# Performance work log

Hardware: AMD Instinct MI355X
Metric: run time of the kernel (lower is better)

The kernel has to match this reference:

```python
import jax, jax.numpy as jnp
import numpy as np

EPSILON = 1e-08

def setup_inputs() -> dict:
    key0 = jax.random.key(0)
    kq, kk, kv = jax.random.split(key0, 3)
    B, Q, H, D = 64, 16, 1, 64
    KV, DV = 16384, 64
    query = jax.random.normal(kq, (B, Q, H, D), dtype=jnp.float32)
    key = jax.random.normal(kk, (B, KV, H, D), dtype=jnp.float32)
    value = jax.random.normal(kv, (B, KV, H, DV), dtype=jnp.float32)
    return {"query": query, "key": key, "value": value}

def reference(query, key, value):
    # InvertedDotProductAttention(norm_type='mean', multi_head=False)
    d = query.shape[-1]
    q = query / jnp.sqrt(jnp.asarray(d, dtype=query.dtype))
    # logits: [b, h, q, k]
    attn = jnp.einsum('bqhd,bkhd->bhqk', q, key)
    # inverted attention: softmax over the query axis (-2)
    attn = jax.nn.softmax(attn, axis=-2)
    # renormalize_keys=True (norm_type == 'mean'): normalize over key axis
    attn = attn / (jnp.sum(attn, axis=-1, keepdims=True) + EPSILON)
    out = jnp.einsum('bhqk,bkhd->bqhd', attn, value)
    # multi_head=False -> squeeze the (singleton) heads axis
    return jnp.squeeze(out, axis=-2)
```

## Files before the change

kernel.cpp:

```cpp
#include <hip/hip_runtime.h>

namespace {

typedef float f32x4 __attribute__((ext_vector_type(4)));
typedef short bf16x8 __attribute__((ext_vector_type(8)));

constexpr int Bn = 64, QN = 16, Dn = 64, DVn = 64, KVn = 16384;
constexpr int MAX_SPLITS = 32;
constexpr int TILE    = 64;
constexpr int THREADS = 256;
constexpr int AP   = 68;
constexpr int VROW = 160;

constexpr float SCALE = 0.125f * 1.4426950408889634f;

__device__ __forceinline__ unsigned cvt_pk_bf16(float a, float b) {
    unsigned r;
    asm("v_cvt_pk_bf16_f32 %0, %1, %2" : "=v"(r) : "v"(a), "v"(b));
    return r;
}

union FragU { unsigned u[4]; bf16x8 v; };

__device__ __forceinline__ void split8(const float x[8], bf16x8& hi, bf16x8& lo) {
    FragU uh, ul;
#pragma unroll
    for (int p = 0; p < 4; ++p) {
        const float a = x[2 * p], b2 = x[2 * p + 1];
        const unsigned h = cvt_pk_bf16(a, b2);
        uh.u[p] = h;
        const float ha = __uint_as_float(h << 16);
        const float hb = __uint_as_float(h & 0xffff0000u);
        ul.u[p] = cvt_pk_bf16(a - ha, b2 - hb);
    }
    hi = uh.v; lo = ul.v;
}

__global__ __launch_bounds__(THREADS, 4)
void inv_attn_part(const float* __restrict__ query,
                   const float* __restrict__ key,
                   const float* __restrict__ value,
                   float* __restrict__ pout,
                   float* __restrict__ pden,
                   int ntiles)
{
    __shared__ __align__(16) float a_s[2][QN * AP];
    __shared__ __align__(16) char  vT[2][DVn * VROW];
    __shared__ float den_buf[4][QN];

    const int tid  = threadIdx.x;
    const int lane = tid & 63;
    const int w    = tid >> 6;
    const int l15  = lane & 15;
    const int g    = lane >> 4;
    const int spl  = blockIdx.x;
    const int splits = gridDim.x;
    const int b    = blockIdx.y;
    const int kt0  = spl * ntiles * TILE;

    bf16x8 qhi[2], qlo[2];
    {
        const float* qp = query + ((size_t)b * QN + l15) * Dn + g * 8;
#pragma unroll
        for (int ks = 0; ks < 2; ++ks) {
            const float4 u0 = *reinterpret_cast<const float4*>(qp + ks * 32);
            const float4 u1 = *reinterpret_cast<const float4*>(qp + ks * 32 + 4);
            float x[8] = { u0.x * SCALE, u0.y * SCALE, u0.z * SCALE, u0.w * SCALE,
                           u1.x * SCALE, u1.y * SCALE, u1.z * SCALE, u1.w * SCALE };
            split8(x, qhi[ks], qlo[ks]);
        }
    }

    f32x4 oacc = {0.f, 0.f, 0.f, 0.f};
    float den0 = 0.f, den1 = 0.f, den2 = 0.f, den3 = 0.f;

    const int vkey = tid >> 4;
    const int vdv0 = (tid & 15) * 4;
    const int vsw  = ((tid & 15) & 7) << 4;

    const float* kbase = key   + ((size_t)b * KVn + kt0 + w * 16 + l15) * Dn + g * 8;
    const float* vbase = value + ((size_t)b * KVn + kt0 + vkey) * Dn + vdv0;

    for (int t = 0; t < ntiles; ++t) {
        const int buf = t & 1;

        float4 vv[4];
#pragma unroll
        for (int i = 0; i < 4; ++i)
            vv[i] = *reinterpret_cast<const float4*>(vbase + ((size_t)t * TILE + 16 * i) * Dn);
#pragma unroll
        for (int i = 0; i < 4; ++i) {
            const int kk = vkey + 16 * i;
#pragma unroll
            for (int j = 0; j < 4; ++j) {
                const float xv = (j == 0) ? vv[i].x : (j == 1) ? vv[i].y
                                : (j == 2) ? vv[i].z : vv[i].w;
                const unsigned uu = cvt_pk_bf16(xv, xv);
                *reinterpret_cast<short*>(&vT[buf][(vdv0 + j) * VROW + ((2 * kk) ^ vsw)]) =
                    (short)uu;
            }
        }

        f32x4 sacc = {0.f, 0.f, 0.f, 0.f};
#pragma unroll
        for (int ks = 0; ks < 2; ++ks) {
            const float4 ka = *reinterpret_cast<const float4*>(kbase + (size_t)t * TILE * Dn + ks * 32);
            const float4 kb = *reinterpret_cast<const float4*>(kbase + (size_t)t * TILE * Dn + ks * 32 + 4);
            float x[8] = { ka.x, ka.y, ka.z, ka.w, kb.x, kb.y, kb.z, kb.w };
            bf16x8 khi, klo;
            split8(x, khi, klo);
            sacc = __builtin_amdgcn_mfma_f32_16x16x32_bf16(qhi[ks], khi, sacc, 0, 0, 0);
            sacc = __builtin_amdgcn_mfma_f32_16x16x32_bf16(qhi[ks], klo, sacc, 0, 0, 0);
            sacc = __builtin_amdgcn_mfma_f32_16x16x32_bf16(qlo[ks], khi, sacc, 0, 0, 0);
        }

        float m = fmaxf(fmaxf(sacc[0], sacc[1]), fmaxf(sacc[2], sacc[3]));
        m = fmaxf(m, __shfl_xor(m, 16, 64));
        m = fmaxf(m, __shfl_xor(m, 32, 64));
        float p0 = exp2f(sacc[0] - m), p1 = exp2f(sacc[1] - m);
        float p2 = exp2f(sacc[2] - m), p3 = exp2f(sacc[3] - m);
        float s4 = p0 + p1 + p2 + p3;
        s4 += __shfl_xor(s4, 16, 64);
        s4 += __shfl_xor(s4, 32, 64);
        const float inv = 1.0f / s4;
        p0 *= inv; p1 *= inv; p2 *= inv; p3 *= inv;
        const int kloc = w * 16 + l15;
        a_s[buf][(g * 4 + 0) * AP + kloc] = p0;
        a_s[buf][(g * 4 + 1) * AP + kloc] = p1;
        a_s[buf][(g * 4 + 2) * AP + kloc] = p2;
        a_s[buf][(g * 4 + 3) * AP + kloc] = p3;
        den0 += p0; den1 += p1; den2 += p2; den3 += p3;

        __syncthreads();

#pragma unroll
        for (int ks = 0; ks < 2; ++ks) {
            const int base = ks * 32 + g * 8;
            const float4 a0 = *reinterpret_cast<const float4*>(&a_s[buf][l15 * AP + base]);
            const float4 a1 = *reinterpret_cast<const float4*>(&a_s[buf][l15 * AP + base + 4]);
            FragU ua;
            ua.u[0] = cvt_pk_bf16(a0.x, a0.y);
            ua.u[1] = cvt_pk_bf16(a0.z, a0.w);
            ua.u[2] = cvt_pk_bf16(a1.x, a1.y);
            ua.u[3] = cvt_pk_bf16(a1.z, a1.w);
            const int dv = w * 16 + l15;
            const int gran = (((ks * 4 + g) ^ ((dv >> 2) & 7)) << 4);
            const bf16x8 vf = *reinterpret_cast<const bf16x8*>(&vT[buf][dv * VROW + gran]);
            oacc = __builtin_amdgcn_mfma_f32_16x16x32_bf16(ua.v, vf, oacc, 0, 0, 0);
        }
    }

    const size_t obase = (((size_t)b * splits + spl) * QN) * DVn;
    const int dv = w * 16 + l15;
    pout[obase + (g * 4 + 0) * DVn + dv] = oacc[0];
    pout[obase + (g * 4 + 1) * DVn + dv] = oacc[1];
    pout[obase + (g * 4 + 2) * DVn + dv] = oacc[2];
    pout[obase + (g * 4 + 3) * DVn + dv] = oacc[3];

#pragma unroll
    for (int off = 1; off < 16; off <<= 1) {
        den0 += __shfl_xor(den0, off, 64);
        den1 += __shfl_xor(den1, off, 64);
        den2 += __shfl_xor(den2, off, 64);
        den3 += __shfl_xor(den3, off, 64);
    }
    if (l15 == 0) {
        den_buf[w][g * 4 + 0] = den0;
        den_buf[w][g * 4 + 1] = den1;
        den_buf[w][g * 4 + 2] = den2;
        den_buf[w][g * 4 + 3] = den3;
    }
    __syncthreads();
    if (tid < QN) {
        const float d = den_buf[0][tid] + den_buf[1][tid] + den_buf[2][tid] + den_buf[3][tid];
        pden[((size_t)b * splits + spl) * QN + tid] = d;
    }
}

__global__ __launch_bounds__(256)
void inv_attn_reduce(const float* __restrict__ pout,
                     const float* __restrict__ pden,
                     float* __restrict__ out,
                     int splits)
{
    const int gid = blockIdx.x * blockDim.x + threadIdx.x;
    const int dv = gid & 63;
    const int q  = (gid >> 6) & (QN - 1);
    const int b  = gid >> 10;
    float sum = 0.f, den = 0.f;
#pragma unroll 8
    for (int sp = 0; sp < splits; ++sp) {
        sum += pout[(((size_t)b * splits + sp) * QN + q) * DVn + dv];
        den += pden[((size_t)b * splits + sp) * QN + q];
    }
    out[gid] = sum / (den + 1e-8f);
}

}

extern "C" void kernel_launch(void* const* d_in, const int* in_sizes, int n_in,
                              void* d_out, int out_size, void* d_ws, size_t ws_size,
                              hipStream_t stream) {
    const float* query = (const float*)d_in[0];
    const float* key   = (const float*)d_in[1];
    const float* value = (const float*)d_in[2];
    float* out = (float*)d_out;

    int splits = MAX_SPLITS;
    auto need = [](int s) {
        return (size_t)Bn * s * QN * DVn * sizeof(float)
             + (size_t)Bn * s * QN * sizeof(float);
    };
    while (splits > 1 && need(splits) > ws_size) splits >>= 1;

    float* pout = (float*)d_ws;
    float* pden = pout + (size_t)Bn * splits * QN * DVn;

    const int ntiles = KVn / (splits * TILE);

    dim3 grid1(splits, Bn);
    inv_attn_part<<<grid1, THREADS, 0, stream>>>(query, key, value, pout, pden, ntiles);

    const int total = Bn * QN * DVn;
    inv_attn_reduce<<<total / 256, 256, 0, stream>>>(pout, pden, out, splits);
}
```

Baseline: 105.5 us.

## Make each wave process independent key tiles and drop block-wide barriers

Each wavefront now handles its own pair of 16-key groups per iteration and computes P·V with only a per-wave LDS transpose of the probabilities. V is loaded straight from global memory in MFMA fragment layout, which removes the shared V transpose and the per-tile __syncthreads. Per-wave partial outputs and denominators are written out, so the reduce kernel sums four times as many partials. This removes barrier and LDS staging costs, but the V loads become strided scalar loads and the partial-buffer traffic grows.

Measured after the change: 123.8 us. 17.3% more time.

```diff
diff --git a/kernel.cpp b/kernel.cpp
--- a/kernel.cpp
+++ b/kernel.cpp
@@ -7,10 +7,9 @@
 
 constexpr int Bn = 64, QN = 16, Dn = 64, DVn = 64, KVn = 16384;
 constexpr int MAX_SPLITS = 32;
-constexpr int TILE    = 64;
+constexpr int TILE = 64;
 constexpr int THREADS = 256;
-constexpr int AP   = 68;
-constexpr int VROW = 160;
+constexpr int PTP = 20;
 
 constexpr float SCALE = 0.125f * 1.4426950408889634f;
 
@@ -22,18 +21,47 @@
 
 union FragU { unsigned u[4]; bf16x8 v; };
 
-__device__ __forceinline__ void split8(const float x[8], bf16x8& hi, bf16x8& lo) {
+__device__ __forceinline__ void split8(const float* x, bf16x8& hi, bf16x8& lo) {
     FragU uh, ul;
 #pragma unroll
     for (int p = 0; p < 4; ++p) {
-        const float a = x[2 * p], b2 = x[2 * p + 1];
-        const unsigned h = cvt_pk_bf16(a, b2);
+        const float a = x[2 * p], b = x[2 * p + 1];
+        const unsigned h = cvt_pk_bf16(a, b);
         uh.u[p] = h;
         const float ha = __uint_as_float(h << 16);
         const float hb = __uint_as_float(h & 0xffff0000u);
-        ul.u[p] = cvt_pk_bf16(a - ha, b2 - hb);
+        ul.u[p] = cvt_pk_bf16(a - ha, b - hb);
     }
     hi = uh.v; lo = ul.v;
+}
+
+__device__ __forceinline__ f32x4 qk_softmax(const float* kp,
+                                            const bf16x8 qhi[2],
+                                            const bf16x8 qlo[2]) {
+    f32x4 sacc = {0.f, 0.f, 0.f, 0.f};
+#pragma unroll
+    for (int ks = 0; ks < 2; ++ks) {
+        const float4 a = *reinterpret_cast<const float4*>(kp + ks * 32);
+        const float4 b = *reinterpret_cast<const float4*>(kp + ks * 32 + 4);
+        float x[8] = {a.x, a.y, a.z, a.w, b.x, b.y, b.z, b.w};
+        bf16x8 khi, klo;
+        split8(x, khi, klo);
+        sacc = __builtin_amdgcn_mfma_f32_16x16x32_bf16(qhi[ks], khi, sacc, 0, 0, 0);
+        sacc = __builtin_amdgcn_mfma_f32_16x16x32_bf16(qhi[ks], klo, sacc, 0, 0, 0);
+        sacc = __builtin_amdgcn_mfma_f32_16x16x32_bf16(qlo[ks], khi, sacc, 0, 0, 0);
+    }
+    float m = fmaxf(fmaxf(sacc[0], sacc[1]), fmaxf(sacc[2], sacc[3]));
+    m = fmaxf(m, __shfl_xor(m, 16, 64));
+    m = fmaxf(m, __shfl_xor(m, 32, 64));
+    f32x4 pr;
+    pr[0] = exp2f(sacc[0] - m); pr[1] = exp2f(sacc[1] - m);
+    pr[2] = exp2f(sacc[2] - m); pr[3] = exp2f(sacc[3] - m);
+    float s = pr[0] + pr[1] + pr[2] + pr[3];
+    s += __shfl_xor(s, 16, 64);
+    s += __shfl_xor(s, 32, 64);
+    const float inv = 1.0f / s;
+    pr[0] *= inv; pr[1] *= inv; pr[2] *= inv; pr[3] *= inv;
+    return pr;
 }
 
 __global__ __launch_bounds__(THREADS, 4)
@@ -42,21 +70,19 @@
                    const float* __restrict__ value,
                    float* __restrict__ pout,
                    float* __restrict__ pden,
-                   int ntiles)
+                   int npairs)
 {
-    __shared__ __align__(16) float a_s[2][QN * AP];
-    __shared__ __align__(16) char  vT[2][DVn * VROW];
-    __shared__ float den_buf[4][QN];
-
-    const int tid  = threadIdx.x;
+    __shared__ __align__(16) float pT[4][32 * PTP];
+
+    const int tid = threadIdx.x;
     const int lane = tid & 63;
-    const int w    = tid >> 6;
-    const int l15  = lane & 15;
-    const int g    = lane >> 4;
-    const int spl  = blockIdx.x;
+    const int w = tid >> 6;
+    const int l15 = lane & 15;
+    const int g = lane >> 4;
+    const int spl = blockIdx.x;
     const int splits = gridDim.x;
-    const int b    = blockIdx.y;
-    const int kt0  = spl * ntiles * TILE;
+    const int b = blockIdx.y;
+    const int kt0 = spl * (npairs * 2 * TILE) + w * 16;
 
     bf16x8 qhi[2], qlo[2];
     {
@@ -65,115 +91,82 @@
         for (int ks = 0; ks < 2; ++ks) {
             const float4 u0 = *reinterpret_cast<const float4*>(qp + ks * 32);
             const float4 u1 = *reinterpret_cast<const float4*>(qp + ks * 32 + 4);
-            float x[8] = { u0.x * SCALE, u0.y * SCALE, u0.z * SCALE, u0.w * SCALE,
-                           u1.x * SCALE, u1.y * SCALE, u1.z * SCALE, u1.w * SCALE };
+            float x[8] = {u0.x * SCALE, u0.y * SCALE, u0.z * SCALE, u0.w * SCALE,
+                          u1.x * SCALE, u1.y * SCALE, u1.z * SCALE, u1.w * SCALE};
             split8(x, qhi[ks], qlo[ks]);
         }
     }
 
-    f32x4 oacc = {0.f, 0.f, 0.f, 0.f};
-    float den0 = 0.f, den1 = 0.f, den2 = 0.f, den3 = 0.f;
-
-    const int vkey = tid >> 4;
-    const int vdv0 = (tid & 15) * 4;
-    const int vsw  = ((tid & 15) & 7) << 4;
-
-    const float* kbase = key   + ((size_t)b * KVn + kt0 + w * 16 + l15) * Dn + g * 8;
-    const float* vbase = value + ((size_t)b * KVn + kt0 + vkey) * Dn + vdv0;
-
-    for (int t = 0; t < ntiles; ++t) {
-        const int buf = t & 1;
-
-        float4 vv[4];
-#pragma unroll
-        for (int i = 0; i < 4; ++i)
-            vv[i] = *reinterpret_cast<const float4*>(vbase + ((size_t)t * TILE + 16 * i) * Dn);
-#pragma unroll
-        for (int i = 0; i < 4; ++i) {
-            const int kk = vkey + 16 * i;
-#pragma unroll
-            for (int j = 0; j < 4; ++j) {
-                const float xv = (j == 0) ? vv[i].x : (j == 1) ? vv[i].y
-                                : (j == 2) ? vv[i].z : vv[i].w;
-                const unsigned uu = cvt_pk_bf16(xv, xv);
-                *reinterpret_cast<short*>(&vT[buf][(vdv0 + j) * VROW + ((2 * kk) ^ vsw)]) =
-                    (short)uu;
-            }
-        }
-
-        f32x4 sacc = {0.f, 0.f, 0.f, 0.f};
-#pragma unroll
-        for (int ks = 0; ks < 2; ++ks) {
-            const float4 ka = *reinterpret_cast<const float4*>(kbase + (size_t)t * TILE * Dn + ks * 32);
-            const float4 kb = *reinterpret_cast<const float4*>(kbase + (size_t)t * TILE * Dn + ks * 32 + 4);
-            float x[8] = { ka.x, ka.y, ka.z, ka.w, kb.x, kb.y, kb.z, kb.w };
-            bf16x8 khi, klo;
-            split8(x, khi, klo);
-            sacc = __builtin_amdgcn_mfma_f32_16x16x32_bf16(qhi[ks], khi, sacc, 0, 0, 0);
-            sacc = __builtin_amdgcn_mfma_f32_16x16x32_bf16(qhi[ks], klo, sacc, 0, 0, 0);
-            sacc = __builtin_amdgcn_mfma_f32_16x16x32_bf16(qlo[ks], khi, sacc, 0, 0, 0);
-        }
-
-        float m = fmaxf(fmaxf(sacc[0], sacc[1]), fmaxf(sacc[2], sacc[3]));
-        m = fmaxf(m, __shfl_xor(m, 16, 64));
-        m = fmaxf(m, __shfl_xor(m, 32, 64));
-        float p0 = exp2f(sacc[0] - m), p1 = exp2f(sacc[1] - m);
-        float p2 = exp2f(sacc[2] - m), p3 = exp2f(sacc[3] - m);
-        float s4 = p0 + p1 + p2 + p3;
-        s4 += __shfl_xor(s4, 16, 64);
-        s4 += __shfl_xor(s4, 32, 64);
-        const float inv = 1.0f / s4;
-        p0 *= inv; p1 *= inv; p2 *= inv; p3 *= inv;
-        const int kloc = w * 16 + l15;
-        a_s[buf][(g * 4 + 0) * AP + kloc] = p0;
-        a_s[buf][(g * 4 + 1) * AP + kloc] = p1;
-        a_s[buf][(g * 4 + 2) * AP + kloc] = p2;
-        a_s[buf][(g * 4 + 3) * AP + kloc] = p3;
-        den0 += p0; den1 += p1; den2 += p2; den3 += p3;
-
-        __syncthreads();
-
-#pragma unroll
-        for (int ks = 0; ks < 2; ++ks) {
-            const int base = ks * 32 + g * 8;
-            const float4 a0 = *reinterpret_cast<const float4*>(&a_s[buf][l15 * AP + base]);
-            const float4 a1 = *reinterpret_cast<const float4*>(&a_s[buf][l15 * AP + base + 4]);
-            FragU ua;
-            ua.u[0] = cvt_pk_bf16(a0.x, a0.y);
-            ua.u[1] = cvt_pk_bf16(a0.z, a0.w);
-            ua.u[2] = cvt_pk_bf16(a1.x, a1.y);
-            ua.u[3] = cvt_pk_bf16(a1.z, a1.w);
-            const int dv = w * 16 + l15;
-            const int gran = (((ks * 4 + g) ^ ((dv >> 2) & 7)) << 4);
-            const bf16x8 vf = *reinterpret_cast<const bf16x8*>(&vT[buf][dv * VROW + gran]);
-            oacc = __builtin_amdgcn_mfma_f32_16x16x32_bf16(ua.v, vf, oacc, 0, 0, 0);
-        }
-    }
-
-    const size_t obase = (((size_t)b * splits + spl) * QN) * DVn;
-    const int dv = w * 16 + l15;
-    pout[obase + (g * 4 + 0) * DVn + dv] = oacc[0];
-    pout[obase + (g * 4 + 1) * DVn + dv] = oacc[1];
-    pout[obase + (g * 4 + 2) * DVn + dv] = oacc[2];
-    pout[obase + (g * 4 + 3) * DVn + dv] = oacc[3];
+    const float* kp = key + ((size_t)b * KVn + kt0 + l15) * Dn + g * 8;
+    const float* vp = value + ((size_t)b * KVn + kt0 + (g & 1) * 8 + (g >> 1) * TILE) * Dn + l15;
+    float* pTw = &pT[w][0];
+
+    f32x4 o0 = {0.f,0.f,0.f,0.f}, o1 = {0.f,0.f,0.f,0.f},
+          o2 = {0.f,0.f,0.f,0.f}, o3 = {0.f,0.f,0.f,0.f};
+    f32x4 den = {0.f,0.f,0.f,0.f};
+
+    for (int p = 0; p < npairs; ++p) {
+        const f32x4 pA = qk_softmax(kp, qhi, qlo);
+        const f32x4 pB = qk_softmax(kp + 64 * Dn, qhi, qlo);
+        den[0] += pA[0] + pB[0]; den[1] += pA[1] + pB[1];
+        den[2] += pA[2] + pB[2]; den[3] += pA[3] + pB[3];
+
+        *reinterpret_cast<f32x4*>(&pTw[l15 * PTP + g * 4]) = pA;
+        *reinterpret_cast<f32x4*>(&pTw[(16 + l15) * PTP + g * 4]) = pB;
+
+        float ax[8];
+#pragma unroll
+        for (int j = 0; j < 8; ++j) ax[j] = pTw[(g * 8 + j) * PTP + l15];
+        FragU ua;
+        ua.u[0] = cvt_pk_bf16(ax[0], ax[1]);
+        ua.u[1] = cvt_pk_bf16(ax[2], ax[3]);
+        ua.u[2] = cvt_pk_bf16(ax[4], ax[5]);
+        ua.u[3] = cvt_pk_bf16(ax[6], ax[7]);
+
+#define PV_CHUNK(c, oc) {                                                     \
+        float vx[8];                                                          \
+        _Pragma("unroll")                                                     \
+        for (int j = 0; j < 8; ++j) vx[j] = vp[j * Dn + (c) * 16];            \
+        FragU uv;                                                             \
+        uv.u[0] = cvt_pk_bf16(vx[0], vx[1]);                                  \
+        uv.u[1] = cvt_pk_bf16(vx[2], vx[3]);                                  \
+        uv.u[2] = cvt_pk_bf16(vx[4], vx[5]);                                  \
+        uv.u[3] = cvt_pk_bf16(vx[6], vx[7]);                                  \
+        oc = __builtin_amdgcn_mfma_f32_16x16x32_bf16(ua.v, uv.v, oc, 0, 0, 0); }
+        PV_CHUNK(0, o0)
+        PV_CHUNK(1, o1)
+        PV_CHUNK(2, o2)
+        PV_CHUNK(3, o3)
+#undef PV_CHUNK
+
+        kp += 128 * Dn;
+        vp += 128 * Dn;
+    }
+
+    const int s4 = spl * 4 + w;
+    const size_t obase = (((size_t)b * (splits * 4) + s4) * QN) * DVn;
+#pragma unroll
+    for (int r = 0; r < 4; ++r) {
+        const int q = g * 4 + r;
+        pout[obase + q * DVn +  0 + l15] = o0[r];
+        pout[obase + q * DVn + 16 + l15] = o1[r];
+        pout[obase + q * DVn + 32 + l15] = o2[r];
+        pout[obase + q * DVn + 48 + l15] = o3[r];
+    }
 
 #pragma unroll
     for (int off = 1; off < 16; off <<= 1) {
-        den0 += __shfl_xor(den0, off, 64);
-        den1 += __shfl_xor(den1, off, 64);
-        den2 += __shfl_xor(den2, off, 64);
-        den3 += __shfl_xor(den3, off, 64);
+        den[0] += __shfl_xor(den[0], off, 64);
+        den[1] += __shfl_xor(den[1], off, 64);
+        den[2] += __shfl_xor(den[2], off, 64);
+        den[3] += __shfl_xor(den[3], off, 64);
     }
     if (l15 == 0) {
-        den_buf[w][g * 4 + 0] = den0;
-        den_buf[w][g * 4 + 1] = den1;
-        den_buf[w][g * 4 + 2] = den2;
-        den_buf[w][g * 4 + 3] = den3;
-    }
-    __syncthreads();
-    if (tid < QN) {
-        const float d = den_buf[0][tid] + den_buf[1][tid] + den_buf[2][tid] + den_buf[3][tid];
-        pden[((size_t)b * splits + spl) * QN + tid] = d;
+        const size_t dbase = ((size_t)b * (splits * 4) + s4) * QN + g * 4;
+        pden[dbase + 0] = den[0];
+        pden[dbase + 1] = den[1];
+        pden[dbase + 2] = den[2];
+        pden[dbase + 3] = den[3];
     }
 }
 
@@ -181,17 +174,17 @@
 void inv_attn_reduce(const float* __restrict__ pout,
                      const float* __restrict__ pden,
                      float* __restrict__ out,
-                     int splits)
+                     int splits4)
 {
     const int gid = blockIdx.x * blockDim.x + threadIdx.x;
     const int dv = gid & 63;
     const int q  = (gid >> 6) & (QN - 1);
     const int b  = gid >> 10;
     float sum = 0.f, den = 0.f;
-#pragma unroll 8
-    for (int sp = 0; sp < splits; ++sp) {
-        sum += pout[(((size_t)b * splits + sp) * QN + q) * DVn + dv];
-        den += pden[((size_t)b * splits + sp) * QN + q];
+#pragma unroll 4
+    for (int sp = 0; sp < splits4; ++sp) {
+        sum += pout[(((size_t)b * splits4 + sp) * QN + q) * DVn + dv];
+        den += pden[((size_t)b * splits4 + sp) * QN + q];
     }
     out[gid] = sum / (den + 1e-8f);
 }
@@ -208,19 +201,19 @@
 
     int splits = MAX_SPLITS;
     auto need = [](int s) {
-        return (size_t)Bn * s * QN * DVn * sizeof(float)
-             + (size_t)Bn * s * QN * sizeof(float);
+        return (size_t)Bn * s * 4 * QN * DVn * sizeof(float)
+             + (size_t)Bn * s * 4 * QN * sizeof(float);
     };
     while (splits > 1 && need(splits) > ws_size) splits >>= 1;
 
     float* pout = (float*)d_ws;
-    float* pden = pout + (size_t)Bn * splits * QN * DVn;
-
-    const int ntiles = KVn / (splits * TILE);
+    float* pden = pout + (size_t)Bn * (splits * 4) * QN * DVn;
+
+    const int npairs = KVn / (splits * TILE * 2);
 
     dim3 grid1(splits, Bn);
-    inv_attn_part<<<grid1, THREADS, 0, stream>>>(query, key, value, pout, pden, ntiles);
+    inv_attn_part<<<grid1, THREADS, 0, stream>>>(query, key, value, pout, pden, npairs);
 
     const int total = Bn * QN * DVn;
-    inv_attn_reduce<<<total / 256, 256, 0, stream>>>(pout, pden, out, splits);
-}
+    inv_attn_reduce<<<total / 256, 256, 0, stream>>>(pout, pden, out, splits * 4);
+}
```

## Prefetch next K/V tile into registers and write per-wave partial denominators

Applied to the files above, without the earlier changes.

The main loop now loads the next tile's key and value float4s into a second register set before the current tile's QK MFMA and softmax, alternating two register buffers through a two-way unrolled loop. This hides global-load latency behind compute. The block-level denominator reduction (shared buffer plus a final __syncthreads) is replaced by each wave writing its own partial sums. The reduce kernel sums four times as many denominator entries. Register pressure rises with the duplicated K/V buffers, and the unroll assumes ntiles is even.

New measurement: 121.2 us. +14.9%, slower.

```diff
diff --git a/kernel.cpp b/kernel.cpp
--- a/kernel.cpp
+++ b/kernel.cpp
@@ -7,7 +7,7 @@
 
 constexpr int Bn = 64, QN = 16, Dn = 64, DVn = 64, KVn = 16384;
 constexpr int MAX_SPLITS = 32;
-constexpr int TILE    = 64;
+constexpr int TILE = 64;
 constexpr int THREADS = 256;
 constexpr int AP   = 68;
 constexpr int VROW = 160;
@@ -22,16 +22,16 @@
 
 union FragU { unsigned u[4]; bf16x8 v; };
 
-__device__ __forceinline__ void split8(const float x[8], bf16x8& hi, bf16x8& lo) {
+__device__ __forceinline__ void split8(const float* x, bf16x8& hi, bf16x8& lo) {
     FragU uh, ul;
 #pragma unroll
     for (int p = 0; p < 4; ++p) {
-        const float a = x[2 * p], b2 = x[2 * p + 1];
-        const unsigned h = cvt_pk_bf16(a, b2);
+        const float a = x[2 * p], b = x[2 * p + 1];
+        const unsigned h = cvt_pk_bf16(a, b);
         uh.u[p] = h;
         const float ha = __uint_as_float(h << 16);
         const float hb = __uint_as_float(h & 0xffff0000u);
-        ul.u[p] = cvt_pk_bf16(a - ha, b2 - hb);
+        ul.u[p] = cvt_pk_bf16(a - ha, b - hb);
     }
     hi = uh.v; lo = ul.v;
 }
@@ -46,7 +46,6 @@
 {
     __shared__ __align__(16) float a_s[2][QN * AP];
     __shared__ __align__(16) char  vT[2][DVn * VROW];
-    __shared__ float den_buf[4][QN];
 
     const int tid  = threadIdx.x;
     const int lane = tid & 63;
@@ -65,48 +64,61 @@
         for (int ks = 0; ks < 2; ++ks) {
             const float4 u0 = *reinterpret_cast<const float4*>(qp + ks * 32);
             const float4 u1 = *reinterpret_cast<const float4*>(qp + ks * 32 + 4);
-            float x[8] = { u0.x * SCALE, u0.y * SCALE, u0.z * SCALE, u0.w * SCALE,
-                           u1.x * SCALE, u1.y * SCALE, u1.z * SCALE, u1.w * SCALE };
+            float x[8] = {u0.x * SCALE, u0.y * SCALE, u0.z * SCALE, u0.w * SCALE,
+                          u1.x * SCALE, u1.y * SCALE, u1.z * SCALE, u1.w * SCALE};
             split8(x, qhi[ks], qlo[ks]);
         }
     }
 
-    f32x4 oacc = {0.f, 0.f, 0.f, 0.f};
-    float den0 = 0.f, den1 = 0.f, den2 = 0.f, den3 = 0.f;
-
+    const float* kbase = key + ((size_t)b * KVn + kt0 + w * 16 + l15) * Dn + g * 8;
     const int vkey = tid >> 4;
     const int vdv0 = (tid & 15) * 4;
     const int vsw  = ((tid & 15) & 7) << 4;
-
-    const float* kbase = key   + ((size_t)b * KVn + kt0 + w * 16 + l15) * Dn + g * 8;
     const float* vbase = value + ((size_t)b * KVn + kt0 + vkey) * Dn + vdv0;
 
-    for (int t = 0; t < ntiles; ++t) {
-        const int buf = t & 1;
-
-        float4 vv[4];
-#pragma unroll
-        for (int i = 0; i < 4; ++i)
-            vv[i] = *reinterpret_cast<const float4*>(vbase + ((size_t)t * TILE + 16 * i) * Dn);
+    f32x4 oacc = {0.f, 0.f, 0.f, 0.f};
+    f32x4 den  = {0.f, 0.f, 0.f, 0.f};
+
+    float4 kA[4], vA[4], kB[4], vB[4];
+#pragma unroll
+    for (int h = 0; h < 4; ++h)
+        kA[h] = *reinterpret_cast<const float4*>(kbase + (h >> 1) * 32 + (h & 1) * 4);
+#pragma unroll
+    for (int i = 0; i < 4; ++i)
+        vA[i] = *reinterpret_cast<const float4*>(vbase + (size_t)(16 * i) * Dn);
+
+    auto body = [&](int t, int buf, float4 (&kc)[4], float4 (&vc)[4],
+                    float4 (&kn)[4], float4 (&vn)[4]) {
 #pragma unroll
         for (int i = 0; i < 4; ++i) {
             const int kk = vkey + 16 * i;
 #pragma unroll
             for (int j = 0; j < 4; ++j) {
-                const float xv = (j == 0) ? vv[i].x : (j == 1) ? vv[i].y
-                                : (j == 2) ? vv[i].z : vv[i].w;
-                const unsigned uu = cvt_pk_bf16(xv, xv);
-                *reinterpret_cast<short*>(&vT[buf][(vdv0 + j) * VROW + ((2 * kk) ^ vsw)]) =
-                    (short)uu;
+                const float xv = (j == 0) ? vc[i].x : (j == 1) ? vc[i].y
+                                : (j == 2) ? vc[i].z : vc[i].w;
+                *reinterpret_cast<short*>(
+                    &vT[buf][(vdv0 + j) * VROW + ((2 * kk) ^ vsw)]) =
+                    (short)cvt_pk_bf16(xv, xv);
             }
         }
 
+        if (t + 1 < ntiles) {
+            const size_t koff = (size_t)(t + 1) * TILE * Dn;
+#pragma unroll
+            for (int h = 0; h < 4; ++h)
+                kn[h] = *reinterpret_cast<const float4*>(
+                    kbase + koff + (h >> 1) * 32 + (h & 1) * 4);
+#pragma unroll
+            for (int i = 0; i < 4; ++i)
+                vn[i] = *reinterpret_cast<const float4*>(
+                    vbase + koff + (size_t)(16 * i) * Dn);
+        }
+
         f32x4 sacc = {0.f, 0.f, 0.f, 0.f};
 #pragma unroll
         for (int ks = 0; ks < 2; ++ks) {
-            const float4 ka = *reinterpret_cast<const float4*>(kbase + (size_t)t * TILE * Dn + ks * 32);
-            const float4 kb = *reinterpret_cast<const float4*>(kbase + (size_t)t * TILE * Dn + ks * 32 + 4);
-            float x[8] = { ka.x, ka.y, ka.z, ka.w, kb.x, kb.y, kb.z, kb.w };
+            const float4 a = kc[ks * 2], c = kc[ks * 2 + 1];
+            float x[8] = {a.x, a.y, a.z, a.w, c.x, c.y, c.z, c.w};
             bf16x8 khi, klo;
             split8(x, khi, klo);
             sacc = __builtin_amdgcn_mfma_f32_16x16x32_bf16(qhi[ks], khi, sacc, 0, 0, 0);
@@ -119,17 +131,17 @@
         m = fmaxf(m, __shfl_xor(m, 32, 64));
         float p0 = exp2f(sacc[0] - m), p1 = exp2f(sacc[1] - m);
         float p2 = exp2f(sacc[2] - m), p3 = exp2f(sacc[3] - m);
-        float s4 = p0 + p1 + p2 + p3;
-        s4 += __shfl_xor(s4, 16, 64);
-        s4 += __shfl_xor(s4, 32, 64);
-        const float inv = 1.0f / s4;
+        float s = p0 + p1 + p2 + p3;
+        s += __shfl_xor(s, 16, 64);
+        s += __shfl_xor(s, 32, 64);
+        const float inv = 1.0f / s;
         p0 *= inv; p1 *= inv; p2 *= inv; p3 *= inv;
         const int kloc = w * 16 + l15;
         a_s[buf][(g * 4 + 0) * AP + kloc] = p0;
         a_s[buf][(g * 4 + 1) * AP + kloc] = p1;
         a_s[buf][(g * 4 + 2) * AP + kloc] = p2;
         a_s[buf][(g * 4 + 3) * AP + kloc] = p3;
-        den0 += p0; den1 += p1; den2 += p2; den3 += p3;
+        den[0] += p0; den[1] += p1; den[2] += p2; den[3] += p3;
 
         __syncthreads();
 
@@ -148,32 +160,32 @@
             const bf16x8 vf = *reinterpret_cast<const bf16x8*>(&vT[buf][dv * VROW + gran]);
             oacc = __builtin_amdgcn_mfma_f32_16x16x32_bf16(ua.v, vf, oacc, 0, 0, 0);
         }
+    };
+
+    for (int t = 0; t < ntiles; t += 2) {
+        body(t,     0, kA, vA, kB, vB);
+        body(t + 1, 1, kB, vB, kA, vA);
     }
 
     const size_t obase = (((size_t)b * splits + spl) * QN) * DVn;
     const int dv = w * 16 + l15;
-    pout[obase + (g * 4 + 0) * DVn + dv] = oacc[0];
-    pout[obase + (g * 4 + 1) * DVn + dv] = oacc[1];
-    pout[obase + (g * 4 + 2) * DVn + dv] = oacc[2];
-    pout[obase + (g * 4 + 3) * DVn + dv] = oacc[3];
+#pragma unroll
+    for (int r = 0; r < 4; ++r)
+        pout[obase + (g * 4 + r) * DVn + dv] = oacc[r];
 
 #pragma unroll
     for (int off = 1; off < 16; off <<= 1) {
-        den0 += __shfl_xor(den0, off, 64);
-        den1 += __shfl_xor(den1, off, 64);
-        den2 += __shfl_xor(den2, off, 64);
-        den3 += __shfl_xor(den3, off, 64);
+        den[0] += __shfl_xor(den[0], off, 64);
+        den[1] += __shfl_xor(den[1], off, 64);
+        den[2] += __shfl_xor(den[2], off, 64);
+        den[3] += __shfl_xor(den[3], off, 64);
     }
     if (l15 == 0) {
-        den_buf[w][g * 4 + 0] = den0;
-        den_buf[w][g * 4 + 1] = den1;
-        den_buf[w][g * 4 + 2] = den2;
-        den_buf[w][g * 4 + 3] = den3;
-    }
-    __syncthreads();
-    if (tid < QN) {
-        const float d = den_buf[0][tid] + den_buf[1][tid] + den_buf[2][tid] + den_buf[3][tid];
-        pden[((size_t)b * splits + spl) * QN + tid] = d;
+        const size_t dbase = ((size_t)b * (splits * 4) + spl * 4 + w) * QN + g * 4;
+        pden[dbase + 0] = den[0];
+        pden[dbase + 1] = den[1];
+        pden[dbase + 2] = den[2];
+        pden[dbase + 3] = den[3];
     }
 }
 
@@ -188,11 +200,12 @@
     const int q  = (gid >> 6) & (QN - 1);
     const int b  = gid >> 10;
     float sum = 0.f, den = 0.f;
-#pragma unroll 8
-    for (int sp = 0; sp < splits; ++sp) {
+#pragma unroll 4
+    for (int sp = 0; sp < splits; ++sp)
         sum += pout[(((size_t)b * splits + sp) * QN + q) * DVn + dv];
-        den += pden[((size_t)b * splits + sp) * QN + q];
-    }
+#pragma unroll 4
+    for (int sp = 0; sp < splits * 4; ++sp)
+        den += pden[((size_t)b * splits * 4 + sp) * QN + q];
     out[gid] = sum / (den + 1e-8f);
 }
 
@@ -209,7 +222,7 @@
     int splits = MAX_SPLITS;
     auto need = [](int s) {
         return (size_t)Bn * s * QN * DVn * sizeof(float)
-             + (size_t)Bn * s * QN * sizeof(float);
+             + (size_t)Bn * s * 4 * QN * sizeof(float);
     };
     while (splits > 1 && need(splits) > ws_size) splits >>= 1;
 
```

## Stream K/V tiles via async global-to-LDS loads with double buffering, fewer splits

Applied to the files above, without the earlier changes.

Replaces the register-staged K/V loads and bf16 transposed V store with direct global_load_lds copies into swizzled, double-buffered fp32 LDS tiles, prefetching the next tile while the current one is computed. V fragments are now gathered element-wise from LDS and converted to bf16 at use. The split count is fixed at 8 (from up to 32), which gives 512 blocks, and occupancy is lowered to 2 blocks per CU because of the larger LDS footprint. This risks lower parallelism for a bandwidth-bound kernel and more LDS read traffic per tile, and it drops the workspace-size check.

Result: faster. 102.3 us (median of 2 runs) (-3.1%).

```diff
diff --git a/kernel.cpp b/kernel.cpp
--- a/kernel.cpp
+++ b/kernel.cpp
@@ -6,11 +6,11 @@
 typedef short bf16x8 __attribute__((ext_vector_type(8)));
 
 constexpr int Bn = 64, QN = 16, Dn = 64, DVn = 64, KVn = 16384;
-constexpr int MAX_SPLITS = 32;
+constexpr int SPLITS  = 8;
 constexpr int TILE    = 64;
 constexpr int THREADS = 256;
-constexpr int AP   = 68;
-constexpr int VROW = 160;
+constexpr int NT      = KVn / (SPLITS * TILE);
+constexpr int AP      = 68;
 
 constexpr float SCALE = 0.125f * 1.4426950408889634f;
 
@@ -22,7 +22,7 @@
 
 union FragU { unsigned u[4]; bf16x8 v; };
 
-__device__ __forceinline__ void split8(const float x[8], bf16x8& hi, bf16x8& lo) {
+__device__ __forceinline__ void split8(const float* x, bf16x8& hi, bf16x8& lo) {
     FragU uh, ul;
 #pragma unroll
     for (int p = 0; p < 4; ++p) {
@@ -36,16 +36,23 @@
     hi = uh.v; lo = ul.v;
 }
 
-__global__ __launch_bounds__(THREADS, 4)
+__device__ __forceinline__ void gl_lds16(const float* g, float* l) {
+    __builtin_amdgcn_global_load_lds(
+        (const __attribute__((address_space(1))) unsigned int*)g,
+        (__attribute__((address_space(3))) unsigned int*)l,
+        16, 0, 0);
+}
+
+__global__ __launch_bounds__(THREADS, 2)
 void inv_attn_part(const float* __restrict__ query,
                    const float* __restrict__ key,
                    const float* __restrict__ value,
                    float* __restrict__ pout,
-                   float* __restrict__ pden,
-                   int ntiles)
+                   float* __restrict__ pden)
 {
+    __shared__ __align__(16) float kbuf[2][TILE * Dn];
+    __shared__ __align__(16) float vbuf[2][TILE * DVn];
     __shared__ __align__(16) float a_s[2][QN * AP];
-    __shared__ __align__(16) char  vT[2][DVn * VROW];
     __shared__ float den_buf[4][QN];
 
     const int tid  = threadIdx.x;
@@ -54,9 +61,8 @@
     const int l15  = lane & 15;
     const int g    = lane >> 4;
     const int spl  = blockIdx.x;
-    const int splits = gridDim.x;
     const int b    = blockIdx.y;
-    const int kt0  = spl * ntiles * TILE;
+    const int kt0  = spl * NT * TILE;
 
     bf16x8 qhi[2], qlo[2];
     {
@@ -65,8 +71,8 @@
         for (int ks = 0; ks < 2; ++ks) {
             const float4 u0 = *reinterpret_cast<const float4*>(qp + ks * 32);
             const float4 u1 = *reinterpret_cast<const float4*>(qp + ks * 32 + 4);
-            float x[8] = { u0.x * SCALE, u0.y * SCALE, u0.z * SCALE, u0.w * SCALE,
-                           u1.x * SCALE, u1.y * SCALE, u1.z * SCALE, u1.w * SCALE };
+            float x[8] = {u0.x * SCALE, u0.y * SCALE, u0.z * SCALE, u0.w * SCALE,
+                          u1.x * SCALE, u1.y * SCALE, u1.z * SCALE, u1.w * SCALE};
             split8(x, qhi[ks], qlo[ks]);
         }
     }
@@ -74,39 +80,42 @@
     f32x4 oacc = {0.f, 0.f, 0.f, 0.f};
     float den0 = 0.f, den1 = 0.f, den2 = 0.f, den3 = 0.f;
 
-    const int vkey = tid >> 4;
-    const int vdv0 = (tid & 15) * 4;
-    const int vsw  = ((tid & 15) & 7) << 4;
-
-    const float* kbase = key   + ((size_t)b * KVn + kt0 + w * 16 + l15) * Dn + g * 8;
-    const float* vbase = value + ((size_t)b * KVn + kt0 + vkey) * Dn + vdv0;
-
-    for (int t = 0; t < ntiles; ++t) {
+    const int srow   = lane >> 4;
+    const int schunk = lane & 15;
+    const float* kg = key   + ((size_t)b * KVn + kt0) * Dn;
+    const float* vg = value + ((size_t)b * KVn + kt0) * Dn;
+
+    auto issue_tile = [&](int t, int buf) {
+#pragma unroll
+        for (int i = 0; i < 4; ++i) {
+            const int r  = w * 16 + i * 4 + srow;
+            const int sc = schunk ^ (r & 7);
+            const size_t off = (size_t)(t * TILE + r) * Dn + sc * 4;
+            gl_lds16(kg + off, &kbuf[buf][(w * 16 + i * 4) * Dn]);
+            gl_lds16(vg + off, &vbuf[buf][(w * 16 + i * 4) * DVn]);
+        }
+    };
+
+    issue_tile(0, 0);
+
+    for (int t = 0; t < NT; ++t) {
         const int buf = t & 1;
 
-        float4 vv[4];
-#pragma unroll
-        for (int i = 0; i < 4; ++i)
-            vv[i] = *reinterpret_cast<const float4*>(vbase + ((size_t)t * TILE + 16 * i) * Dn);
-#pragma unroll
-        for (int i = 0; i < 4; ++i) {
-            const int kk = vkey + 16 * i;
-#pragma unroll
-            for (int j = 0; j < 4; ++j) {
-                const float xv = (j == 0) ? vv[i].x : (j == 1) ? vv[i].y
-                                : (j == 2) ? vv[i].z : vv[i].w;
-                const unsigned uu = cvt_pk_bf16(xv, xv);
-                *reinterpret_cast<short*>(&vT[buf][(vdv0 + j) * VROW + ((2 * kk) ^ vsw)]) =
-                    (short)uu;
-            }
-        }
-
+        __syncthreads();
+
+        if (t + 1 < NT) issue_tile(t + 1, buf ^ 1);
+
+        const int rq = w * 16 + l15;
+        const int sw = rq & 7;
         f32x4 sacc = {0.f, 0.f, 0.f, 0.f};
 #pragma unroll
         for (int ks = 0; ks < 2; ++ks) {
-            const float4 ka = *reinterpret_cast<const float4*>(kbase + (size_t)t * TILE * Dn + ks * 32);
-            const float4 kb = *reinterpret_cast<const float4*>(kbase + (size_t)t * TILE * Dn + ks * 32 + 4);
-            float x[8] = { ka.x, ka.y, ka.z, ka.w, kb.x, kb.y, kb.z, kb.w };
+            const int c0 = ks * 8 + g * 2;
+            const f32x4 r0 = *reinterpret_cast<const f32x4*>(
+                &kbuf[buf][rq * Dn + ((c0    ) ^ sw) * 4]);
+            const f32x4 r1 = *reinterpret_cast<const f32x4*>(
+                &kbuf[buf][rq * Dn + ((c0 + 1) ^ sw) * 4]);
+            float x[8] = {r0[0], r0[1], r0[2], r0[3], r1[0], r1[1], r1[2], r1[3]};
             bf16x8 khi, klo;
             split8(x, khi, klo);
             sacc = __builtin_amdgcn_mfma_f32_16x16x32_bf16(qhi[ks], khi, sacc, 0, 0, 0);
@@ -124,15 +133,16 @@
         s4 += __shfl_xor(s4, 32, 64);
         const float inv = 1.0f / s4;
         p0 *= inv; p1 *= inv; p2 *= inv; p3 *= inv;
-        const int kloc = w * 16 + l15;
-        a_s[buf][(g * 4 + 0) * AP + kloc] = p0;
-        a_s[buf][(g * 4 + 1) * AP + kloc] = p1;
-        a_s[buf][(g * 4 + 2) * AP + kloc] = p2;
-        a_s[buf][(g * 4 + 3) * AP + kloc] = p3;
+        a_s[buf][(g * 4 + 0) * AP + rq] = p0;
+        a_s[buf][(g * 4 + 1) * AP + rq] = p1;
+        a_s[buf][(g * 4 + 2) * AP + rq] = p2;
+        a_s[buf][(g * 4 + 3) * AP + rq] = p3;
         den0 += p0; den1 += p1; den2 += p2; den3 += p3;
 
         __syncthreads();
 
+        const int dv = w * 16 + l15;
+        const int ch = dv >> 2, wrd = dv & 3;
 #pragma unroll
         for (int ks = 0; ks < 2; ++ks) {
             const int base = ks * 32 + g * 8;
@@ -143,19 +153,27 @@
             ua.u[1] = cvt_pk_bf16(a0.z, a0.w);
             ua.u[2] = cvt_pk_bf16(a1.x, a1.y);
             ua.u[3] = cvt_pk_bf16(a1.z, a1.w);
-            const int dv = w * 16 + l15;
-            const int gran = (((ks * 4 + g) ^ ((dv >> 2) & 7)) << 4);
-            const bf16x8 vf = *reinterpret_cast<const bf16x8*>(&vT[buf][dv * VROW + gran]);
-            oacc = __builtin_amdgcn_mfma_f32_16x16x32_bf16(ua.v, vf, oacc, 0, 0, 0);
-        }
-    }
-
-    const size_t obase = (((size_t)b * splits + spl) * QN) * DVn;
-    const int dv = w * 16 + l15;
-    pout[obase + (g * 4 + 0) * DVn + dv] = oacc[0];
-    pout[obase + (g * 4 + 1) * DVn + dv] = oacc[1];
-    pout[obase + (g * 4 + 2) * DVn + dv] = oacc[2];
-    pout[obase + (g * 4 + 3) * DVn + dv] = oacc[3];
+            float vx[8];
+#pragma unroll
+            for (int j = 0; j < 8; ++j) {
+                const int k = base + j;
+                vx[j] = vbuf[buf][k * DVn + ((ch ^ j) << 2) + wrd];
+            }
+            FragU uv;
+            uv.u[0] = cvt_pk_bf16(vx[0], vx[1]);
+            uv.u[1] = cvt_pk_bf16(vx[2], vx[3]);
+            uv.u[2] = cvt_pk_bf16(vx[4], vx[5]);
+            uv.u[3] = cvt_pk_bf16(vx[6], vx[7]);
+            oacc = __builtin_amdgcn_mfma_f32_16x16x32_bf16(ua.v, uv.v, oacc, 0, 0, 0);
+        }
+    }
+
+    const size_t obase = (((size_t)b * SPLITS + spl) * QN) * DVn;
+    const int dvo = w * 16 + l15;
+    pout[obase + (g * 4 + 0) * DVn + dvo] = oacc[0];
+    pout[obase + (g * 4 + 1) * DVn + dvo] = oacc[1];
+    pout[obase + (g * 4 + 2) * DVn + dvo] = oacc[2];
+    pout[obase + (g * 4 + 3) * DVn + dvo] = oacc[3];
 
 #pragma unroll
     for (int off = 1; off < 16; off <<= 1) {
@@ -173,15 +191,14 @@
     __syncthreads();
     if (tid < QN) {
         const float d = den_buf[0][tid] + den_buf[1][tid] + den_buf[2][tid] + den_buf[3][tid];
-        pden[((size_t)b * splits + spl) * QN + tid] = d;
+        pden[((size_t)b * SPLITS + spl) * QN + tid] = d;
     }
 }
 
 __global__ __launch_bounds__(256)
 void inv_attn_reduce(const float* __restrict__ pout,
                      const float* __restrict__ pden,
-                     float* __restrict__ out,
-                     int splits)
+                     float* __restrict__ out)
 {
     const int gid = blockIdx.x * blockDim.x + threadIdx.x;
     const int dv = gid & 63;
@@ -189,9 +206,9 @@
     const int b  = gid >> 10;
     float sum = 0.f, den = 0.f;
 #pragma unroll 8
-    for (int sp = 0; sp < splits; ++sp) {
-        sum += pout[(((size_t)b * splits + sp) * QN + q) * DVn + dv];
-        den += pden[((size_t)b * splits + sp) * QN + q];
+    for (int sp = 0; sp < SPLITS; ++sp) {
+        sum += pout[(((size_t)b * SPLITS + sp) * QN + q) * DVn + dv];
+        den += pden[((size_t)b * SPLITS + sp) * QN + q];
     }
     out[gid] = sum / (den + 1e-8f);
 }
@@ -206,21 +223,12 @@
     const float* value = (const float*)d_in[2];
     float* out = (float*)d_out;
 
-    int splits = MAX_SPLITS;
-    auto need = [](int s) {
-        return (size_t)Bn * s * QN * DVn * sizeof(float)
-             + (size_t)Bn * s * QN * sizeof(float);
-    };
-    while (splits > 1 && need(splits) > ws_size) splits >>= 1;
-
     float* pout = (float*)d_ws;
-    float* pden = pout + (size_t)Bn * splits * QN * DVn;
-
-    const int ntiles = KVn / (splits * TILE);
-
-    dim3 grid1(splits, Bn);
-    inv_attn_part<<<grid1, THREADS, 0, stream>>>(query, key, value, pout, pden, ntiles);
+    float* pden = pout + (size_t)Bn * SPLITS * QN * DVn;
+
+    dim3 grid1(SPLITS, Bn);
+    inv_attn_part<<<grid1, THREADS, 0, stream>>>(query, key, value, pout, pden);
 
     const int total = Bn * QN * DVn;
-    inv_attn_reduce<<<total / 256, 256, 0, stream>>>(pout, pden, out, splits);
-}
+    inv_attn_reduce<<<total / 256, 256, 0, stream>>>(pout, pden, out);
+}
```
